# Kernel tuning notes

Hardware: AMD Instinct MI355X
Metric: run time of the kernel (lower is better)

Reference implementation:

```python
import jax, jax.numpy as jnp
import numpy as np

N = 200000      # nodes
E = 1600000     # directed edges (before self-loops)
G = 5000        # graphs (molecules)
IN, HID, OUT, HEADS = 128, 128, 128, 3


def gat_layer(x, src, dst, W, a_src, a_dst, b, heads, out_dim, concat):
    n = x.shape[0]
    h = (x @ W).reshape(n, heads, out_dim)                 # [N,H,F]
    al_s = jnp.einsum('nhf,hf->nh', h, a_src)              # [N,H]
    al_d = jnp.einsum('nhf,hf->nh', h, a_dst)
    e = jax.nn.leaky_relu(al_s[src] + al_d[dst], 0.2)      # [E,H]
    m = jax.ops.segment_max(e, dst, num_segments=n)        # softmax over incoming edges
    ex = jnp.exp(e - m[dst])
    den = jax.ops.segment_sum(ex, dst, num_segments=n)
    alpha = ex / (den[dst] + 1e-16)                        # [E,H]
    msg = h[src] * alpha[..., None]                        # [E,H,F]
    agg = jax.ops.segment_sum(msg, dst, num_segments=n)    # [N,H,F]
    agg = agg.reshape(n, heads * out_dim) if concat else agg.mean(axis=1)
    return agg + b


def setup_inputs() -> dict:
    key = jax.random.key(0)
    ks = jax.random.split(key, 16)
    d = {}
    d['x'] = jax.random.normal(ks[0], (N, IN), dtype=jnp.float32)
    d['edge_index'] = jax.random.randint(ks[1], (2, E), 0, N, dtype=jnp.int64)
    d['batch'] = jnp.sort(jax.random.randint(ks[2], (N,), 0, G, dtype=jnp.int64))
    s = 0.1
    d['W1'] = jax.random.normal(ks[3], (IN, HEADS * HID), jnp.float32) * s
    d['a1s'] = jax.random.normal(ks[4], (HEADS, HID), jnp.float32) * s
    d['a1d'] = jax.random.normal(ks[5], (HEADS, HID), jnp.float32) * s
    d['b1'] = jnp.zeros((HEADS * HID,), jnp.float32)
    d['W2'] = jax.random.normal(ks[6], (HEADS * HID, HEADS * HID), jnp.float32) * s
    d['a2s'] = jax.random.normal(ks[7], (HEADS, HID), jnp.float32) * s
    d['a2d'] = jax.random.normal(ks[8], (HEADS, HID), jnp.float32) * s
    d['b2'] = jnp.zeros((HEADS * HID,), jnp.float32)
    d['W3'] = jax.random.normal(ks[9], (HEADS * HID, OUT), jnp.float32) * s
    d['a3s'] = jax.random.normal(ks[10], (1, OUT), jnp.float32) * s
    d['a3d'] = jax.random.normal(ks[11], (1, OUT), jnp.float32) * s
    d['b3'] = jnp.zeros((OUT,), jnp.float32)
    return d


def reference(x, edge_index, batch, W1, a1s, a1d, b1, W2, a2s, a2d, b2, W3, a3s, a3d, b3):
    # PyG GATConv default add_self_loops=True
    loops = jnp.arange(N, dtype=edge_index.dtype)
    src = jnp.concatenate([edge_index[0], loops])
    dst = jnp.concatenate([edge_index[1], loops])
    h = jax.nn.leaky_relu(gat_layer(x, src, dst, W1, a1s, a1d, b1, HEADS, HID, True), 0.2)
    h = jax.nn.leaky_relu(gat_layer(h, src, dst, W2, a2s, a2d, b2, HEADS, HID, True), 0.2)
    h = jax.nn.leaky_relu(gat_layer(h, src, dst, W3, a3s, a3d, b3, 1, OUT, False), 0.2)
    # global mean pool over graphs
    sums = jax.ops.segment_sum(h, batch, num_segments=G)            # [G,OUT]
    cnt = jax.ops.segment_sum(jnp.ones((N,), h.dtype), batch, num_segments=G)
    return sums / jnp.maximum(cnt, 1.0)[:, None]
```

## Files before the change

kernel.cpp:

```cpp
#include <hip/hip_runtime.h>
#include <hip/hip_bf16.h>
#include <math.h>

#define LRELU_SLOPE 0.2f
typedef __hip_bfloat16 bf16;
typedef __hip_bfloat162 bf16x2;

typedef short s8v __attribute__((ext_vector_type(8)));
typedef short s4v __attribute__((ext_vector_type(4)));
typedef float f4v __attribute__((ext_vector_type(4)));

__device__ __forceinline__ float lrelu(float v) { return v > 0.f ? v : LRELU_SLOPE * v; }
__device__ __forceinline__ float b2f(short b) {
  return __uint_as_float(((unsigned)(unsigned short)b) << 16);
}

__device__ __forceinline__ void st2(float* p, float x, float y) {
  *(float2*)p = float2{x, y};
}

template <typename T>
__device__ __forceinline__ void nt_store16(void* p, T v) {
  union { T t; unsigned long long q[2]; } u;
  u.t = v;
  __builtin_nontemporal_store(u.q[0], (unsigned long long*)p);
  __builtin_nontemporal_store(u.q[1], (unsigned long long*)p + 1);
}


__global__ void k_zero(unsigned int* __restrict__ p, long n) {
  long i = (long)blockIdx.x * blockDim.x + threadIdx.x;
  if (i < n) p[i] = 0u;
}

__global__ void k_zero_out(float* __restrict__ out, int n) {
  int i = blockIdx.x * blockDim.x + threadIdx.x;
  if (i < n) out[i] = 0.f;
}


__global__ void k_cvt(const float* __restrict__ x, bf16* __restrict__ xb, long n) {
  long i = (long)blockIdx.x * blockDim.x + threadIdx.x;
  if (i < n) xb[i] = __float2bfloat16(x[i]);
}

__global__ void k_tw2(const float* __restrict__ W, bf16* __restrict__ B2, int K, int NN) {
  int tid = blockIdx.x * blockDim.x + threadIdx.x;
  int total = (K * NN) >> 3;
  if (tid >= total) return;
  int f = tid >> 6, l = tid & 63;
  int nfr = NN >> 4;
  int k32 = f / nfr, bnG = f - k32 * nfr;
  int col = bnG * 16 + (l & 15);
  int krow = k32 * 32 + (l >> 4) * 8;
  s8v v;
#pragma unroll
  for (int j = 0; j < 8; ++j) {
    bf16 b = __float2bfloat16(W[(size_t)(krow + j) * NN + col]);
    v[j] = *(short*)&b;
  }
  *(s8v*)&B2[(size_t)tid * 8] = v;
}


__global__ void k_hist(const int* __restrict__ dst, int* __restrict__ deg, int E, int Et) {
  int e = blockIdx.x * blockDim.x + threadIdx.x;
  if (e >= Et) return;
  int d = (e < E) ? dst[e] : (e - E);
  atomicAdd(&deg[d], 1);
}

__global__ void k_hist1(const int* __restrict__ idx, int* __restrict__ deg, int n) {
  int i = blockIdx.x * blockDim.x + threadIdx.x;
  if (i < n) atomicAdd(&deg[idx[i]], 1);
}

__global__ void k_scan1(const int* __restrict__ deg, int* __restrict__ offs,
                        int* __restrict__ bsum, int n) {
  __shared__ int sd[256];
  int t = threadIdx.x;
  int base = blockIdx.x * 1024 + t * 4;
  int v[4]; int tsum = 0;
#pragma unroll
  for (int i = 0; i < 4; ++i) { v[i] = (base + i < n) ? deg[base + i] : 0; tsum += v[i]; }
  sd[t] = tsum;
  __syncthreads();
  for (int off = 1; off < 256; off <<= 1) {
    int x = (t >= off) ? sd[t - off] : 0;
    __syncthreads();
    sd[t] += x;
    __syncthreads();
  }
  int excl = sd[t] - tsum;
#pragma unroll
  for (int i = 0; i < 4; ++i) { if (base + i < n) offs[base + i] = excl; excl += v[i]; }
  if (t == 255) bsum[blockIdx.x] = sd[255];
}

__global__ void k_scan2(int* bsum, int nb) {
  if (threadIdx.x == 0 && blockIdx.x == 0) {
    int run = 0;
    for (int i = 0; i < nb; ++i) { int t = bsum[i]; bsum[i] = run; run += t; }
  }
}

__global__ void k_scan3(int* __restrict__ offs, const int* __restrict__ bsum, int n, int total) {
  int t = threadIdx.x;
  int base = blockIdx.x * 1024 + t * 4;
  int add = bsum[blockIdx.x];
#pragma unroll
  for (int i = 0; i < 4; ++i) if (base + i < n) offs[base + i] += add;
  if (blockIdx.x == 0 && t == 0) offs[n] = total;
}

__global__ void k_scatter(const int* __restrict__ src, const int* __restrict__ dst,
                          const int* __restrict__ offs, int* __restrict__ cur,
                          int* __restrict__ ssrc, int E, int Et) {
  int e = blockIdx.x * blockDim.x + threadIdx.x;
  if (e >= Et) return;
  int s, d;
  if (e < E) { s = src[e]; d = dst[e]; } else { s = d = e - E; }
  int pos = offs[d] + atomicAdd(&cur[d], 1);
  ssrc[pos] = s;
}


template <int NT>
__global__ __launch_bounds__(512) void k_gemm_d(const bf16* __restrict__ A,
                                                const bf16* __restrict__ B2,
                                                bf16* __restrict__ C,
                                                int K, int NN) {
  int t = threadIdx.x;
  int wv = t >> 6, lane = t & 63;
  int mg = wv >> 2, ng = wv & 3;
  int quad = lane >> 4, l15 = lane & 15;
  size_t bm0 = (size_t)blockIdx.x * 64;
  const bf16* Ap0 = A + (bm0 + mg * 32 + l15) * (size_t)K + quad * 8;
  const bf16* Ap1 = Ap0 + (size_t)16 * K;
  int nfr = NN >> 4;
  const bf16* Bp = B2 + ((size_t)(ng * NT) << 9) + lane * 8;
  size_t fstep = (size_t)nfr << 9;

  f4v acc[2][NT];
#pragma unroll
  for (int ms = 0; ms < 2; ++ms)
#pragma unroll
    for (int bn = 0; bn < NT; ++bn) acc[ms][bn] = f4v{0, 0, 0, 0};

  s8v a0 = *(const s8v*)Ap0;
  s8v a1 = *(const s8v*)Ap1;
  s8v bf[NT];
#pragma unroll
  for (int bn = 0; bn < NT; ++bn) bf[bn] = *(const s8v*)(Bp + bn * 512);

  int nk = K >> 5;
  for (int ik = 0; ik < nk; ++ik) {
    int nx = (ik + 1 < nk) ? ik + 1 : ik;
    s8v na0 = *(const s8v*)(Ap0 + nx * 32);
    s8v na1 = *(const s8v*)(Ap1 + nx * 32);
    s8v nbf[NT];
#pragma unroll
    for (int bn = 0; bn < NT; ++bn)
      nbf[bn] = *(const s8v*)(Bp + nx * fstep + bn * 512);
#pragma unroll
    for (int bn = 0; bn < NT; ++bn)
      acc[0][bn] = __builtin_amdgcn_mfma_f32_16x16x32_bf16(a0, bf[bn], acc[0][bn], 0, 0, 0);
#pragma unroll
    for (int bn = 0; bn < NT; ++bn)
      acc[1][bn] = __builtin_amdgcn_mfma_f32_16x16x32_bf16(a1, bf[bn], acc[1][bn], 0, 0, 0);
    a0 = na0; a1 = na1;
#pragma unroll
    for (int bn = 0; bn < NT; ++bn) bf[bn] = nbf[bn];
  }

#pragma unroll
  for (int ms = 0; ms < 2; ++ms)
#pragma unroll
    for (int bn = 0; bn < NT; ++bn) {
      int coln = (ng * NT + bn) * 16 + l15;
      size_t rbase = bm0 + mg * 32 + ms * 16 + quad * 4;
#pragma unroll
      for (int r = 0; r < 4; ++r)
        C[(rbase + r) * NN + coln] = __float2bfloat16(acc[ms][bn][r]);
    }
}


template <int H>
__global__ void k_al(const bf16* __restrict__ h, const float* __restrict__ as,
                     const float* __restrict__ ad, float* __restrict__ al_s,
                     float* __restrict__ al_d, int N) {
  constexpr int SP = (H > 1) ? 4 : 1;
  int n = (blockIdx.x * blockDim.x + threadIdx.x) >> 6;
  int lane = threadIdx.x & 63;
  if (n >= N) return;
  int hd = lane >> 4;
  bool active = (hd < H);
  int hdc = active ? hd : 0;
  int f8 = (lane & 15) * 8;
  const bf16* hp = h + (size_t)n * (H * 128) + hdc * 128 + f8;
  s8v hv = *(const s8v*)hp;
  float ss = 0.f, sd = 0.f;
#pragma unroll
  for (int i = 0; i < 8; ++i) {
    float v = b2f(hv[i]);
    ss += v * as[hdc * 128 + f8 + i];
    sd += v * ad[hdc * 128 + f8 + i];
  }
#pragma unroll
  for (int off = 8; off; off >>= 1) {
    ss += __shfl_xor(ss, off, 64);
    sd += __shfl_xor(sd, off, 64);
  }
  if (active && (lane & 15) == 0) {
    al_s[n * SP + hd] = ss;
    al_d[n * SP + hd] = sd;
  }
}


template <int CPL> struct HVec;
template <> struct HVec<8> { typedef s8v T; };
template <> struct HVec<4> { typedef s4v T; };

template <int H, typename OT>
__global__ __launch_bounds__(256) void k_attn_agg(const bf16* __restrict__ hbuf,
                           const int* __restrict__ ssrc,
                           const int* __restrict__ offs, const float* __restrict__ al_s,
                           const float* __restrict__ al_d, const float* __restrict__ bias,
                           OT* __restrict__ out, int N) {
  constexpr int SW  = (H > 1) ? 4 : 2;
  constexpr int ROW = H * 128;
  constexpr int CPL = (H > 1) ? 8 : 4;
  constexpr int NL  = ROW / CPL;
  typedef typename HVec<CPL>::T hvec;

  __shared__ __align__(16) float stash[4][64 * SW];
  int n = (blockIdx.x * blockDim.x + threadIdx.x) >> 6;
  int lane = threadIdx.x & 63;
  if (n >= N) return;
  float* st = stash[threadIdx.x >> 6];
  int start = offs[n], end = offs[n + 1];

  float ald[H];
  if constexpr (H > 1) {
    float4 t = *(const float4*)&al_d[(size_t)n * 4];
    ald[0] = t.x; ald[1] = t.y; ald[2] = t.z;
  } else {
    ald[0] = al_d[n];
  }

  bool act = lane < NL;
  int c0 = act ? lane * CPL : 0;
  int hd_l = c0 >> 7;

  float m[H];
  float den = 0.f;
  float acc[CPL];
#pragma unroll
  for (int hd = 0; hd < H; ++hd) m[hd] = -1e30f;
#pragma unroll
  for (int i = 0; i < CPL; ++i) acc[i] = 0.f;

  for (int cb = start; cb < end; cb += 64) {
    int cl = end - cb; if (cl > 64) cl = 64;
    bool el = lane < cl;
    int mys = el ? ssrc[cb + lane] : 0;
    float ev[H];
    if constexpr (H > 1) {
      float4 av = *(const float4*)&al_s[(size_t)mys * 4];
      ev[0] = av.x; ev[1] = av.y; ev[2] = av.z;
    } else {
      ev[0] = al_s[mys];
    }
#pragma unroll
    for (int hd = 0; hd < H; ++hd)
      ev[hd] = el ? lrelu(ev[hd] + ald[hd]) : -1e30f;

    float nm[H];
#pragma unroll
    for (int hd = 0; hd < H; ++hd) {
      float v = ev[hd];
#pragma unroll
      for (int off = 32; off; off >>= 1) v = fmaxf(v, __shfl_xor(v, off, 64));
      nm[hd] = fmaxf(v, m[hd]);
    }
    if (cb > start) {
      float sc[H];
#pragma unroll
      for (int hd = 0; hd < H; ++hd) sc[hd] = __expf(m[hd] - nm[hd]);
      float so = sc[hd_l];
      den *= so;
#pragma unroll
      for (int i = 0; i < CPL; ++i) acc[i] *= so;
    }
#pragma unroll
    for (int hd = 0; hd < H; ++hd) m[hd] = nm[hd];

    float myex[H];
#pragma unroll
    for (int hd = 0; hd < H; ++hd) myex[hd] = el ? __expf(ev[hd] - m[hd]) : 0.f;

    __builtin_amdgcn_wave_barrier();
    if constexpr (H > 1) {
      float4 s4{__int_as_float(mys), myex[0], myex[1], myex[2]};
      *(float4*)&st[lane * 4] = s4;
    } else {
      float2 s2{__int_as_float(mys), myex[0]};
      *(float2*)&st[lane * 2] = s2;
    }
    asm volatile("s_waitcnt lgkmcnt(0)" ::: "memory");
    __builtin_amdgcn_wave_barrier();

    for (int r = 0; r < cl; r += 8) {
      int su[8]; float a[8];
#pragma unroll
      for (int u = 0; u < 8; ++u) {
        if constexpr (H > 1) {
          float4 ed = *(const float4*)&st[(r + u) * 4];
          su[u] = __float_as_int(ed.x);
          a[u] = (hd_l == 0) ? ed.y : ((hd_l == 1) ? ed.z : ed.w);
        } else {
          float2 ed = *(const float2*)&st[(r + u) * 2];
          su[u] = __float_as_int(ed.x);
          a[u] = ed.y;
        }
        den += a[u];
      }
      hvec hv[8];
#pragma unroll
      for (int u = 0; u < 8; ++u)
        hv[u] = *(const hvec*)(hbuf + (size_t)su[u] * ROW + c0);
#pragma unroll
      for (int u = 0; u < 8; ++u)
#pragma unroll
        for (int i = 0; i < CPL; ++i)
          acc[i] += a[u] * b2f(hv[u][i]);
    }
  }

  if (act) {
    float rr = 1.f / (den + 1e-16f);
    OT* op = out + (size_t)n * ROW + c0;
    if constexpr (sizeof(OT) == 2) {
      s8v ov;
#pragma unroll
      for (int i = 0; i < CPL; ++i) {
        float o = lrelu(acc[i] * rr + bias[c0 + i]);
        bf16 b = __float2bfloat16(o);
        ov[i] = *(short*)&b;
      }
      nt_store16(op, ov);
    } else {
      float4 ov;
      ov.x = lrelu(acc[0] * rr + bias[c0 + 0]);
      ov.y = lrelu(acc[1] * rr + bias[c0 + 1]);
      ov.z = lrelu(acc[2] * rr + bias[c0 + 2]);
      ov.w = lrelu(acc[3] * rr + bias[c0 + 3]);
      nt_store16(op, ov);
    }
  }
}


__global__ void k_pool(const float* __restrict__ h, const int* __restrict__ goffs,
                       float* __restrict__ out, int G) {
  int g = (blockIdx.x * blockDim.x + threadIdx.x) >> 6;
  int lane = threadIdx.x & 63;
  if (g >= G) return;
  int s = goffs[g], e = goffs[g + 1];
  float ax = 0.f, ay = 0.f;
  for (int n = s; n < e; ++n) {
    float2 v = *(const float2*)&h[(size_t)n * 128 + lane * 2];
    ax += v.x; ay += v.y;
  }
  float c = fmaxf((float)(e - s), 1.f);
  st2(&out[(size_t)g * 128 + lane * 2], ax / c, ay / c);
}


extern "C" void kernel_launch(void* const* d_in, const int* in_sizes, int n_in,
                              void* d_out, int out_size, void* d_ws, size_t ws_size,
                              hipStream_t stream) {
  const float* x   = (const float*)d_in[0];
  const int*   ei  = (const int*)d_in[1];
  const int*   bat = (const int*)d_in[2];
  const float* W1  = (const float*)d_in[3];
  const float* a1s = (const float*)d_in[4];
  const float* a1d = (const float*)d_in[5];
  const float* b1  = (const float*)d_in[6];
  const float* W2  = (const float*)d_in[7];
  const float* a2s = (const float*)d_in[8];
  const float* a2d = (const float*)d_in[9];
  const float* b2  = (const float*)d_in[10];
  const float* W3  = (const float*)d_in[11];
  const float* a3s = (const float*)d_in[12];
  const float* a3d = (const float*)d_in[13];
  const float* b3  = (const float*)d_in[14];
  float* out = (float*)d_out;

  const int N = in_sizes[2];
  const int E = in_sizes[1] / 2;
  const int Et = E + N;
  const int G = out_size / 128;

  char* p = (char*)d_ws;
  auto carve = [&](size_t bytes) { void* r = (void*)p; p += (bytes + 255) & ~(size_t)255; return r; };
  bf16*  bufA   = (bf16*)carve((size_t)N * 384 * 2);
  bf16*  bufB   = (bf16*)carve((size_t)N * 384 * 2);
  float* al_s   = (float*)carve((size_t)N * 4 * 4);
  float* al_d   = (float*)carve((size_t)N * 4 * 4);
  int*   ssrc   = (int*)carve((size_t)Et * 4);
  int*   offs   = (int*)carve((size_t)(N + 1) * 4);
  int*   deg    = (int*)carve((size_t)N * 4);
  int*   cur    = (int*)carve((size_t)N * 4);
  int*   bsum   = (int*)carve(4096 * 4);
  int*   gdeg   = (int*)carve((size_t)G * 4);
  int*   goffs  = (int*)carve((size_t)(G + 1) * 4);
  bf16*  Wp1    = (bf16*)carve((size_t)384 * 128 * 2);
  bf16*  Wp2    = (bf16*)carve((size_t)384 * 384 * 2);
  bf16*  Wp3    = (bf16*)carve((size_t)128 * 384 * 2);
  size_t need = (size_t)(p - (char*)d_ws);

  if (ws_size < need) {
    k_zero_out<<<(out_size + 255) / 256, 256, 0, stream>>>(out, out_size);
    return;
  }

  const int* esrc = ei;
  const int* edst = ei + E;

  int ebl = (Et + 255) / 256;
  int NB = (N + 1023) / 1024;
  int GB = (G + 1023) / 1024;
  int nodeWaveBlocks = (N * 64 + 255) / 256;
  int gemmBlocks = (N + 63) / 64;

  bf16* xb = bufA;
  k_cvt<<<((long)N * 128 + 255) / 256, 256, 0, stream>>>(x, xb, (long)N * 128);
  k_tw2<<<(128 * 384 / 8 + 255) / 256, 256, 0, stream>>>(W1, Wp1, 128, 384);
  k_tw2<<<(384 * 384 / 8 + 255) / 256, 256, 0, stream>>>(W2, Wp2, 384, 384);
  k_tw2<<<(384 * 128 / 8 + 255) / 256, 256, 0, stream>>>(W3, Wp3, 384, 128);

  k_zero<<<(N + 255) / 256, 256, 0, stream>>>((unsigned int*)deg, N);
  k_hist<<<ebl, 256, 0, stream>>>(edst, deg, E, Et);
  k_scan1<<<NB, 256, 0, stream>>>(deg, offs, bsum, N);
  k_scan2<<<1, 64, 0, stream>>>(bsum, NB);
  k_scan3<<<NB, 256, 0, stream>>>(offs, bsum, N, Et);
  k_zero<<<(N + 255) / 256, 256, 0, stream>>>((unsigned int*)cur, N);
  k_scatter<<<ebl, 256, 0, stream>>>(esrc, edst, offs, cur, ssrc, E, Et);

  k_zero<<<(G + 255) / 256, 256, 0, stream>>>((unsigned int*)gdeg, G);
  k_hist1<<<(N + 255) / 256, 256, 0, stream>>>(bat, gdeg, N);
  k_scan1<<<GB, 256, 0, stream>>>(gdeg, goffs, bsum, G);
  k_scan2<<<1, 64, 0, stream>>>(bsum, GB);
  k_scan3<<<GB, 256, 0, stream>>>(goffs, bsum, G, N);

  k_gemm_d<6><<<gemmBlocks, 512, 0, stream>>>(xb, Wp1, bufB, 128, 384);
  k_al<3><<<nodeWaveBlocks, 256, 0, stream>>>(bufB, a1s, a1d, al_s, al_d, N);
  k_attn_agg<3, bf16><<<nodeWaveBlocks, 256, 0, stream>>>(bufB, ssrc, offs, al_s, al_d, b1, bufA, N);

  k_gemm_d<6><<<gemmBlocks, 512, 0, stream>>>(bufA, Wp2, bufB, 384, 384);
  k_al<3><<<nodeWaveBlocks, 256, 0, stream>>>(bufB, a2s, a2d, al_s, al_d, N);
  k_attn_agg<3, bf16><<<nodeWaveBlocks, 256, 0, stream>>>(bufB, ssrc, offs, al_s, al_d, b2, bufA, N);

  k_gemm_d<2><<<gemmBlocks, 512, 0, stream>>>(bufA, Wp3, bufB, 384, 128);
  k_al<1><<<nodeWaveBlocks, 256, 0, stream>>>(bufB, a3s, a3d, al_s, al_d, N);
  float* out3 = (float*)bufA;
  k_attn_agg<1, float><<<nodeWaveBlocks, 256, 0, stream>>>(bufB, ssrc, offs, al_s, al_d, b3, out3, N);

  k_pool<<<(G * 64 + 255) / 256, 256, 0, stream>>>(out3, goffs, out, G);
}
```

Measured before the change: 1.511 ms.

## Deepen GEMM prefetch, parallelize block-sum scan, use buffer NT stores

The GEMM now takes K and N as template constants, fully unrolls the k-loop and keeps a three-deep register prefetch ring instead of one-step double buffering, to hide global load latency. The single-thread block-sum scan is replaced by a 256-thread wave-shuffle scan when the block count is small. Attention-aggregation output stores switch to inline-asm buffer_store_dwordx4 with nt/sc1 bits. These add register pressure in the GEMM and depend on hand-written buffer descriptors, where a 32-bit byte offset could overflow on large outputs.

After: 1.503 ms. About the same (-0.5%).

```diff
diff --git a/kernel.cpp b/kernel.cpp
--- a/kernel.cpp
+++ b/kernel.cpp
@@ -9,6 +9,8 @@
 typedef short s8v __attribute__((ext_vector_type(8)));
 typedef short s4v __attribute__((ext_vector_type(4)));
 typedef float f4v __attribute__((ext_vector_type(4)));
+typedef int   i4v __attribute__((ext_vector_type(4)));
+typedef unsigned int u4v __attribute__((ext_vector_type(4)));
 
 __device__ __forceinline__ float lrelu(float v) { return v > 0.f ? v : LRELU_SLOPE * v; }
 __device__ __forceinline__ float b2f(short b) {
@@ -19,12 +21,17 @@
   *(float2*)p = float2{x, y};
 }
 
-template <typename T>
-__device__ __forceinline__ void nt_store16(void* p, T v) {
-  union { T t; unsigned long long q[2]; } u;
-  u.t = v;
-  __builtin_nontemporal_store(u.q[0], (unsigned long long*)p);
-  __builtin_nontemporal_store(u.q[1], (unsigned long long*)p + 1);
+__device__ __forceinline__ u4v make_srd(const void* p) {
+  u4v r;
+  unsigned long long a = (unsigned long long)p;
+  r.x = (unsigned)a; r.y = (unsigned)(a >> 32);
+  r.z = 0xFFFFFFFFu;
+  r.w = 0x00020000u;
+  return r;
+}
+__device__ __forceinline__ void bstore16_nt(u4v srd, int byteoff, i4v d) {
+  asm volatile("buffer_store_dwordx4 %0, %1, %2, 0 offen sc1 nt"
+               :: "v"(d), "v"(byteoff), "s"(srd));
 }
 
 
@@ -98,10 +105,28 @@
 }
 
 __global__ void k_scan2(int* bsum, int nb) {
-  if (threadIdx.x == 0 && blockIdx.x == 0) {
-    int run = 0;
-    for (int i = 0; i < nb; ++i) { int t = bsum[i]; bsum[i] = run; run += t; }
-  }
+  int t = threadIdx.x;
+  if (nb > 256) {
+    if (t == 0 && blockIdx.x == 0) {
+      int run = 0;
+      for (int i = 0; i < nb; ++i) { int x = bsum[i]; bsum[i] = run; run += x; }
+    }
+    return;
+  }
+  int v = (t < nb) ? bsum[t] : 0;
+  int lane = t & 63, wv = t >> 6;
+  int s = v;
+#pragma unroll
+  for (int off = 1; off < 64; off <<= 1) {
+    int u = __shfl_up(s, off, 64);
+    if (lane >= off) s += u;
+  }
+  __shared__ int wsum[4];
+  if (lane == 63) wsum[wv] = s;
+  __syncthreads();
+  int add = 0;
+  for (int w = 0; w < wv; ++w) add += wsum[w];
+  if (t < nb) bsum[t] = add + s - v;
 }
 
 __global__ void k_scan3(int* __restrict__ offs, const int* __restrict__ bsum, int n, int total) {
@@ -125,11 +150,11 @@
 }
 
 
-template <int NT>
+template <int NT, int K, int NN>
 __global__ __launch_bounds__(512) void k_gemm_d(const bf16* __restrict__ A,
                                                 const bf16* __restrict__ B2,
-                                                bf16* __restrict__ C,
-                                                int K, int NN) {
+                                                bf16* __restrict__ C) {
+  constexpr int nk = K >> 5;
   int t = threadIdx.x;
   int wv = t >> 6, lane = t & 63;
   int mg = wv >> 2, ng = wv & 3;
@@ -137,9 +162,9 @@
   size_t bm0 = (size_t)blockIdx.x * 64;
   const bf16* Ap0 = A + (bm0 + mg * 32 + l15) * (size_t)K + quad * 8;
   const bf16* Ap1 = Ap0 + (size_t)16 * K;
-  int nfr = NN >> 4;
+  constexpr int nfr = NN >> 4;
   const bf16* Bp = B2 + ((size_t)(ng * NT) << 9) + lane * 8;
-  size_t fstep = (size_t)nfr << 9;
+  constexpr size_t fstep = (size_t)nfr << 9;
 
   f4v acc[2][NT];
 #pragma unroll
@@ -147,31 +172,32 @@
 #pragma unroll
     for (int bn = 0; bn < NT; ++bn) acc[ms][bn] = f4v{0, 0, 0, 0};
 
-  s8v a0 = *(const s8v*)Ap0;
-  s8v a1 = *(const s8v*)Ap1;
-  s8v bf[NT];
-#pragma unroll
-  for (int bn = 0; bn < NT; ++bn) bf[bn] = *(const s8v*)(Bp + bn * 512);
-
-  int nk = K >> 5;
+  s8v pa0[3], pa1[3], pb[3][NT];
+#define GLOAD(ik, sl)                                                        \
+  do {                                                                       \
+    pa0[sl] = *(const s8v*)(Ap0 + (ik) * 32);                                \
+    pa1[sl] = *(const s8v*)(Ap1 + (ik) * 32);                                \
+    _Pragma("unroll")                                                        \
+    for (int bn = 0; bn < NT; ++bn)                                          \
+      pb[sl][bn] = *(const s8v*)(Bp + (ik) * fstep + bn * 512);              \
+  } while (0)
+
+  GLOAD(0, 0);
+  if constexpr (nk > 1) GLOAD(1, 1);
+  if constexpr (nk > 2) GLOAD(2, 2);
+
+#pragma unroll
   for (int ik = 0; ik < nk; ++ik) {
-    int nx = (ik + 1 < nk) ? ik + 1 : ik;
-    s8v na0 = *(const s8v*)(Ap0 + nx * 32);
-    s8v na1 = *(const s8v*)(Ap1 + nx * 32);
-    s8v nbf[NT];
+    const int c = ik % 3;
 #pragma unroll
     for (int bn = 0; bn < NT; ++bn)
-      nbf[bn] = *(const s8v*)(Bp + nx * fstep + bn * 512);
+      acc[0][bn] = __builtin_amdgcn_mfma_f32_16x16x32_bf16(pa0[c], pb[c][bn], acc[0][bn], 0, 0, 0);
 #pragma unroll
     for (int bn = 0; bn < NT; ++bn)
-      acc[0][bn] = __builtin_amdgcn_mfma_f32_16x16x32_bf16(a0, bf[bn], acc[0][bn], 0, 0, 0);
-#pragma unroll
-    for (int bn = 0; bn < NT; ++bn)
-      acc[1][bn] = __builtin_amdgcn_mfma_f32_16x16x32_bf16(a1, bf[bn], acc[1][bn], 0, 0, 0);
-    a0 = na0; a1 = na1;
-#pragma unroll
-    for (int bn = 0; bn < NT; ++bn) bf[bn] = nbf[bn];
-  }
+      acc[1][bn] = __builtin_amdgcn_mfma_f32_16x16x32_bf16(pa1[c], pb[c][bn], acc[1][bn], 0, 0, 0);
+    if (ik + 3 < nk) GLOAD(ik + 3, c);
+  }
+#undef GLOAD
 
 #pragma unroll
   for (int ms = 0; ms < 2; ++ms)
@@ -341,23 +367,24 @@
 
   if (act) {
     float rr = 1.f / (den + 1e-16f);
-    OT* op = out + (size_t)n * ROW + c0;
+    u4v srd = make_srd(out);
+    int boff = (int)(((size_t)n * ROW + c0) * sizeof(OT));
     if constexpr (sizeof(OT) == 2) {
-      s8v ov;
+      union { s8v s; i4v i; } u;
 #pragma unroll
       for (int i = 0; i < CPL; ++i) {
         float o = lrelu(acc[i] * rr + bias[c0 + i]);
         bf16 b = __float2bfloat16(o);
-        ov[i] = *(short*)&b;
+        u.s[i] = *(short*)&b;
       }
-      nt_store16(op, ov);
+      bstore16_nt(srd, boff, u.i);
     } else {
-      float4 ov;
-      ov.x = lrelu(acc[0] * rr + bias[c0 + 0]);
-      ov.y = lrelu(acc[1] * rr + bias[c0 + 1]);
-      ov.z = lrelu(acc[2] * rr + bias[c0 + 2]);
-      ov.w = lrelu(acc[3] * rr + bias[c0 + 3]);
-      nt_store16(op, ov);
+      union { float4 f; i4v i; } u;
+      u.f.x = lrelu(acc[0] * rr + bias[c0 + 0]);
+      u.f.y = lrelu(acc[1] * rr + bias[c0 + 1]);
+      u.f.z = lrelu(acc[2] * rr + bias[c0 + 2]);
+      u.f.w = lrelu(acc[3] * rr + bias[c0 + 3]);
+      bstore16_nt(srd, boff, u.i);
     }
   }
 }
@@ -445,7 +472,7 @@
   k_zero<<<(N + 255) / 256, 256, 0, stream>>>((unsigned int*)deg, N);
   k_hist<<<ebl, 256, 0, stream>>>(edst, deg, E, Et);
   k_scan1<<<NB, 256, 0, stream>>>(deg, offs, bsum, N);
-  k_scan2<<<1, 64, 0, stream>>>(bsum, NB);
+  k_scan2<<<1, 256, 0, stream>>>(bsum, NB);
   k_scan3<<<NB, 256, 0, stream>>>(offs, bsum, N, Et);
   k_zero<<<(N + 255) / 256, 256, 0, stream>>>((unsigned int*)cur, N);
   k_scatter<<<ebl, 256, 0, stream>>>(esrc, edst, offs, cur, ssrc, E, Et);
@@ -453,18 +480,18 @@
   k_zero<<<(G + 255) / 256, 256, 0, stream>>>((unsigned int*)gdeg, G);
   k_hist1<<<(N + 255) / 256, 256, 0, stream>>>(bat, gdeg, N);
   k_scan1<<<GB, 256, 0, stream>>>(gdeg, goffs, bsum, G);
-  k_scan2<<<1, 64, 0, stream>>>(bsum, GB);
+  k_scan2<<<1, 256, 0, stream>>>(bsum, GB);
   k_scan3<<<GB, 256, 0, stream>>>(goffs, bsum, G, N);
 
-  k_gemm_d<6><<<gemmBlocks, 512, 0, stream>>>(xb, Wp1, bufB, 128, 384);
+  k_gemm_d<6, 128, 384><<<gemmBlocks, 512, 0, stream>>>(xb, Wp1, bufB);
   k_al<3><<<nodeWaveBlocks, 256, 0, stream>>>(bufB, a1s, a1d, al_s, al_d, N);
   k_attn_agg<3, bf16><<<nodeWaveBlocks, 256, 0, stream>>>(bufB, ssrc, offs, al_s, al_d, b1, bufA, N);
 
-  k_gemm_d<6><<<gemmBlocks, 512, 0, stream>>>(bufA, Wp2, bufB, 384, 384);
+  k_gemm_d<6, 384, 384><<<gemmBlocks, 512, 0, stream>>>(bufA, Wp2, bufB);
   k_al<3><<<nodeWaveBlocks, 256, 0, stream>>>(bufB, a2s, a2d, al_s, al_d, N);
   k_attn_agg<3, bf16><<<nodeWaveBlocks, 256, 0, stream>>>(bufB, ssrc, offs, al_s, al_d, b2, bufA, N);
 
-  k_gemm_d<2><<<gemmBlocks, 512, 0, stream>>>(bufA, Wp3, bufB, 384, 128);
+  k_gemm_d<2, 384, 128><<<gemmBlocks, 512, 0, stream>>>(bufA, Wp3, bufB);
   k_al<1><<<nodeWaveBlocks, 256, 0, stream>>>(bufB, a3s, a3d, al_s, al_d, N);
   float* out3 = (float*)bufA;
   k_attn_agg<1, float><<<nodeWaveBlocks, 256, 0, stream>>>(bufB, ssrc, offs, al_s, al_d, b3, out3, N);
```
